# Performance work log

Hardware: AMD Instinct MI355X
Metric: run time of the kernel (lower is better)

## Reference

```python
import jax, jax.numpy as jnp
import numpy as np

N = 100000      # num_nodes
E = 1600000     # num_edges (avg degree 16)
EMB = 128       # emb_dim
HID = 128       # hidden_size
REPR = 64       # repr_dim


def setup_inputs() -> dict:
    key = jax.random.key(0)
    k0, k1, k2, k3 = jax.random.split(key, 4)
    edge_index = jax.random.randint(k0, (2, E), 0, N)
    node_emb = jax.random.normal(k1, (N, EMB), jnp.float32) * 0.1
    # GCNConv weights: glorot-like init, bias zeros (PyG default)
    W1 = jax.random.normal(k2, (EMB, HID), jnp.float32) * (1.0 / np.sqrt(EMB))
    b1 = jnp.zeros((HID,), jnp.float32)
    W2 = jax.random.normal(k3, (HID, REPR), jnp.float32) * (1.0 / np.sqrt(HID))
    b2 = jnp.zeros((REPR,), jnp.float32)
    return {"edge_index": edge_index, "node_emb": node_emb,
            "W1": W1, "b1": b1, "W2": W2, "b2": b2}


def reference(edge_index, node_emb, W1, b1, W2, b2):
    # PyG GCNConv: add self-loops, symmetric degree normalization,
    # out = scatter_add(norm * (x W)[src] -> dst) + b
    loops = jnp.arange(N, dtype=edge_index.dtype)
    src = jnp.concatenate([edge_index[0], loops])  # [E+N]
    dst = jnp.concatenate([edge_index[1], loops])
    deg = jax.ops.segment_sum(jnp.ones_like(src, dtype=node_emb.dtype), dst,
                              num_segments=N)
    dinv = jax.lax.rsqrt(deg)  # deg >= 1 thanks to self-loops
    norm = dinv[src] * dinv[dst]  # [E+N]

    def gcn_conv(x, W, b):
        h = x @ W                                   # [N, out]
        msg = norm[:, None] * h[src]                # gather + scale, [E+N, out]
        return jax.ops.segment_sum(msg, dst, num_segments=N) + b

    x = jax.nn.relu(gcn_conv(node_emb, W1, b1))
    # F.dropout(training=False) is identity in eval mode
    return gcn_conv(x, W2, b2)
```

## Files before the change

kernel.cpp:

```cpp
#include <hip/hip_runtime.h>
#include <hip/hip_bf16.h>
#include <stdint.h>


static constexpr int KD = 128;
static constexpr int BSH = 9;
static constexpr int MAXB = 256;
static constexpr int CHUNK = 8192;
static constexpr int CAP = 12288;

typedef short bf16x8 __attribute__((ext_vector_type(8)));
typedef float f32x4  __attribute__((ext_vector_type(4)));
typedef float f32x2  __attribute__((ext_vector_type(2)));

__device__ __forceinline__ unsigned short f2bf(float f) {
    __hip_bfloat16 b = __float2bfloat16(f);
    return *reinterpret_cast<unsigned short*>(&b);
}
__device__ __forceinline__ float bflo(unsigned v) { return __uint_as_float(v << 16); }
__device__ __forceinline__ float bfhi(unsigned v) { return __uint_as_float(v & 0xffff0000u); }
__device__ __forceinline__ unsigned pk2(float lo, float hi) {
    return (unsigned)f2bf(lo) | ((unsigned)f2bf(hi) << 16);
}
__device__ __forceinline__ void accp(f32x2* a, uint4 v) {
    f32x2 t;
    t.x = bflo(v.x); t.y = bfhi(v.x); a[0] += t;
    t.x = bflo(v.y); t.y = bfhi(v.y); a[1] += t;
    t.x = bflo(v.z); t.y = bfhi(v.z); a[2] += t;
    t.x = bflo(v.w); t.y = bfhi(v.w); a[3] += t;
}

__global__ __launch_bounds__(256) void init_misc(const float* __restrict__ W1,
        const float* __restrict__ W2, unsigned short* __restrict__ Wt1,
        unsigned short* __restrict__ Wt2, int* __restrict__ bcur, int nbuck) {
    int t = blockIdx.x * 256 + threadIdx.x;
    if (t < 128 * 128) {
        int k = t >> 7, nn = t & 127;
        Wt1[nn * 128 + k] = f2bf(W1[t]);
    } else if (t < 128 * 128 + 128 * 64) {
        int i = t - 128 * 128;
        int k = i >> 6, nn = i & 63;
        Wt2[nn * 128 + k] = f2bf(W2[i]);
    } else if (t < 128 * 128 + 128 * 64 + MAXB) {
        int b = t - (128 * 128 + 128 * 64);
        bcur[b] = b * CAP;
    }
}

__global__ __launch_bounds__(256) void multisplit(const int* __restrict__ src,
        const int* __restrict__ dst, int* __restrict__ bcur,
        int* __restrict__ packed, int e, int nbuck) {
    __shared__ int cnt[MAXB], lbase[MAXB], wbase[MAXB], vcnt[MAXB], scanbuf[256];
    __shared__ int buf[CHUNK];
    const int t = threadIdx.x;
    const int e0 = blockIdx.x * CHUNK;
    const int m = min(CHUNK, e - e0);

    for (int i = t; i < nbuck; i += 256) cnt[i] = 0;
    __syncthreads();
    for (int i = t; i < m; i += 256) atomicAdd(&cnt[dst[e0 + i] >> BSH], 1);
    __syncthreads();
    int v = (t < nbuck) ? cnt[t] : 0;
    scanbuf[t] = v;
    __syncthreads();
    for (int off = 1; off < 256; off <<= 1) {
        int u = (t >= off) ? scanbuf[t - off] : 0;
        __syncthreads();
        scanbuf[t] += u;
        __syncthreads();
    }
    int excl = scanbuf[t] - v;
    if (t < nbuck) {
        lbase[t] = excl;
        vcnt[t] = v;
        wbase[t] = v ? atomicAdd(&bcur[t], v) : 0;
        cnt[t] = excl;
    }
    __syncthreads();
    for (int i = t; i < m; i += 256) {
        int d = dst[e0 + i], s = src[e0 + i];
        int b = d >> BSH;
        int p = atomicAdd(&cnt[b], 1);
        buf[p] = ((d & ((1 << BSH) - 1)) << 22) | s;
    }
    __syncthreads();
    int wv = t >> 6, ln = t & 63;
    for (int b = wv; b < nbuck; b += 4) {
        int c = vcnt[b], st = lbase[b], g = wbase[b];
        int end = min(c, (b + 1) * CAP - g);
        for (int i = ln; i < end; i += 64) packed[g + i] = buf[st + i];
    }
}

__global__ __launch_bounds__(256) void bucket_build(const int* __restrict__ packed,
        const int* __restrict__ bcur, int* __restrict__ roff, int* __restrict__ degN,
        float* __restrict__ dinv, int* __restrict__ csr, int n) {
    __shared__ int deg[1 << BSH];
    __shared__ int cur[1 << BSH];
    __shared__ int wsum[4];
    const int t = threadIdx.x;
    const int b = blockIdx.x;
    const int nodeBase = b << BSH;
    const int nn = min(1 << BSH, n - nodeBase);
    const int e0 = b * CAP, e1 = bcur[b];

    for (int i = t; i < (1 << BSH); i += 256) deg[i] = 0;
    __syncthreads();
    for (int i = e0 + t; i < e1; i += 256)
        atomicAdd(&deg[(unsigned)packed[i] >> 22], 1);
    __syncthreads();

    const int i0 = t * 2;
    int d0 = deg[i0], d1 = deg[i0 + 1];
    int tsum = d0 + d1;
    int lane = t & 63, wv = t >> 6;
    int v = tsum;
    for (int off = 1; off < 64; off <<= 1) {
        int u = __shfl_up(v, off, 64);
        if (lane >= off) v += u;
    }
    if (lane == 63) wsum[wv] = v;
    __syncthreads();
    int woff = 0;
    for (int i = 0; i < wv; ++i) woff += wsum[i];
    int excl = v - tsum + woff;
    int p0 = excl, p1 = excl + d0;
    cur[i0] = p0; cur[i0 + 1] = p1;
    if (i0 < nn) {
        roff[nodeBase + i0] = e0 + p0;
        degN[nodeBase + i0] = d0;
        dinv[nodeBase + i0] = rsqrtf((float)(d0 + 1));
    }
    if (i0 + 1 < nn) {
        roff[nodeBase + i0 + 1] = e0 + p1;
        degN[nodeBase + i0 + 1] = d1;
        dinv[nodeBase + i0 + 1] = rsqrtf((float)(d1 + 1));
    }
    __syncthreads();

    for (int i = e0 + t; i < e1; i += 256) {
        unsigned pk = (unsigned)packed[i];
        int dl = pk >> 22;
        int s = pk & 0x3FFFFF;
        int slot = atomicAdd(&cur[dl], 1);
        csr[e0 + slot] = s;
    }
}

template<int C, bool XBF>
__global__ __launch_bounds__(256) void gemm_mfma(const void* __restrict__ xv,
        const unsigned short* __restrict__ Wt, const float* __restrict__ dinv,
        unsigned short* __restrict__ out, int n)
{
    constexpr int KP = KD + 8;
    constexpr int WP = 64 + 8;
    __shared__ __align__(16) unsigned short xt[64 * KP];
    __shared__ __align__(16) unsigned short lw[C * WP];
    const int t = threadIdx.x;
    const int w = t >> 6, lane = t & 63;
    const int quad = lane >> 4, l16 = lane & 15;
    const int row0 = blockIdx.x * 64;

    for (int i = t; i < 64 * 32; i += 256) {
        int r = i >> 5, c4 = (i & 31) * 4;
        int row = row0 + r;
        ushort4 pk = make_ushort4(0, 0, 0, 0);
        if (row < n) {
            if constexpr (XBF) {
                pk = *reinterpret_cast<const ushort4*>(
                    &((const unsigned short*)xv)[(size_t)row * KD + c4]);
            } else {
                float4 v = *reinterpret_cast<const float4*>(
                    &((const float*)xv)[(size_t)row * KD + c4]);
                pk.x = f2bf(v.x); pk.y = f2bf(v.y); pk.z = f2bf(v.z); pk.w = f2bf(v.w);
            }
        }
        *reinterpret_cast<ushort4*>(&xt[r * KP + c4]) = pk;
    }

    f32x4 acc[C / 16];
#pragma unroll
    for (int i = 0; i < C / 16; ++i) acc[i] = (f32x4)(0.f);

    for (int h = 0; h < 2; ++h) {
        __syncthreads();
        for (int i = t; i < C * 16; i += 256) {
            int nr = i >> 4, j = (i & 15) * 4;
            *reinterpret_cast<ushort4*>(&lw[nr * WP + j]) =
                *reinterpret_cast<const ushort4*>(&Wt[nr * KD + h * 64 + j]);
        }
        __syncthreads();
#pragma unroll
        for (int kt = 0; kt < 2; ++kt) {
            bf16x8 af = *reinterpret_cast<const bf16x8*>(
                &xt[(w * 16 + l16) * KP + h * 64 + kt * 32 + quad * 8]);
#pragma unroll
            for (int ct = 0; ct < C / 16; ++ct) {
                bf16x8 bfr = *reinterpret_cast<const bf16x8*>(
                    &lw[(ct * 16 + l16) * WP + kt * 32 + quad * 8]);
                acc[ct] = __builtin_amdgcn_mfma_f32_16x16x32_bf16(af, bfr, acc[ct], 0, 0, 0);
            }
        }
    }

#pragma unroll
    for (int j = 0; j < 4; ++j) {
        int row = row0 + w * 16 + quad * 4 + j;
        if (row < n) {
            float s = dinv[row];
#pragma unroll
            for (int ct = 0; ct < C / 16; ++ct)
                out[(size_t)row * C + ct * 16 + l16] = f2bf(acc[ct][j] * s);
        }
    }
}

__global__ __launch_bounds__(256) void gather128(const uint4* __restrict__ H,
        const int* __restrict__ roff, const int* __restrict__ degN,
        const int* __restrict__ csr, const float* __restrict__ dinv,
        const float* __restrict__ b, uint4* __restrict__ out, int n)
{
    int wid = (blockIdx.x * 256 + threadIdx.x) >> 6;
    int lane = threadIdx.x & 63;
    if (wid >= n) return;
    const int qw = lane >> 4, cp = lane & 15;
    const char* Hb = (const char*)H;
    const unsigned cpo = (unsigned)cp * 16u;
    f32x2 a[4], c[4];
#pragma unroll
    for (int i = 0; i < 4; ++i) { a[i] = (f32x2)(0.f); c[i] = (f32x2)(0.f); }
    int e0 = roff[wid], e1 = e0 + degN[wid];
    for (int base = e0; base < e1; base += 64) {
        int m = e1 - base; if (m > 64) m = 64;
        int idx = (lane < m) ? csr[base + lane] : 0;
        int j = 0;
        for (; j + 8 <= m; j += 8) {
            unsigned u0 = (unsigned)__shfl(idx, j + qw);
            unsigned u1 = (unsigned)__shfl(idx, j + 4 + qw);
            uint4 v0 = *(const uint4*)(Hb + ((u0 << 8) + cpo));
            uint4 v1 = *(const uint4*)(Hb + ((u1 << 8) + cpo));
            accp(a, v0);
            accp(c, v1);
        }
        for (; j + 4 <= m; j += 4) {
            unsigned u = (unsigned)__shfl(idx, j + qw);
            uint4 v = *(const uint4*)(Hb + ((u << 8) + cpo));
            accp(a, v);
        }
        int r = m - j;
        if (r) {
            unsigned u = (unsigned)__shfl(idx, min(j + qw, m - 1));
            if (qw < r) {
                uint4 v = *(const uint4*)(Hb + ((u << 8) + cpo));
                accp(a, v);
            }
        }
    }
#pragma unroll
    for (int i = 0; i < 4; ++i) a[i] += c[i];
#pragma unroll
    for (int i = 0; i < 4; ++i) {
        a[i].x += __shfl_xor(a[i].x, 16, 64);
        a[i].x += __shfl_xor(a[i].x, 32, 64);
        a[i].y += __shfl_xor(a[i].y, 16, 64);
        a[i].y += __shfl_xor(a[i].y, 32, 64);
    }
    if (qw == 0) {
        uint4 sv = *(const uint4*)(Hb + (((unsigned)wid << 8) + cpo));
        accp(a, sv);
        float s = dinv[wid];
        float4 b0 = ((const float4*)b)[cp * 2];
        float4 b1 = ((const float4*)b)[cp * 2 + 1];
        float r0 = fmaxf(s * a[0].x + b0.x, 0.f), r1 = fmaxf(s * a[0].y + b0.y, 0.f);
        float r2 = fmaxf(s * a[1].x + b0.z, 0.f), r3 = fmaxf(s * a[1].y + b0.w, 0.f);
        float r4 = fmaxf(s * a[2].x + b1.x, 0.f), r5 = fmaxf(s * a[2].y + b1.y, 0.f);
        float r6 = fmaxf(s * a[3].x + b1.z, 0.f), r7 = fmaxf(s * a[3].y + b1.w, 0.f);
        uint4 o;
        o.x = pk2(r0, r1); o.y = pk2(r2, r3); o.z = pk2(r4, r5); o.w = pk2(r6, r7);
        out[(size_t)wid * 16 + cp] = o;
    }
}

__global__ __launch_bounds__(256) void gather64(const uint4* __restrict__ H,
        const int* __restrict__ roff, const int* __restrict__ degN,
        const int* __restrict__ csr, const float* __restrict__ dinv,
        const float* __restrict__ b, float4* __restrict__ out, int n)
{
    int wid = (blockIdx.x * 256 + threadIdx.x) >> 6;
    int lane = threadIdx.x & 63;
    if (wid >= n) return;
    const int oc = lane >> 3, cp = lane & 7;
    const char* Hb = (const char*)H;
    const unsigned cpo = (unsigned)cp * 16u;
    f32x2 a[4], c[4];
#pragma unroll
    for (int i = 0; i < 4; ++i) { a[i] = (f32x2)(0.f); c[i] = (f32x2)(0.f); }
    int e0 = roff[wid], e1 = e0 + degN[wid];
    for (int base = e0; base < e1; base += 64) {
        int m = e1 - base; if (m > 64) m = 64;
        int idx = (lane < m) ? csr[base + lane] : 0;
        int j = 0;
        for (; j + 16 <= m; j += 16) {
            unsigned u0 = (unsigned)__shfl(idx, j + oc);
            unsigned u1 = (unsigned)__shfl(idx, j + 8 + oc);
            uint4 v0 = *(const uint4*)(Hb + ((u0 << 7) + cpo));
            uint4 v1 = *(const uint4*)(Hb + ((u1 << 7) + cpo));
            accp(a, v0);
            accp(c, v1);
        }
        for (; j + 8 <= m; j += 8) {
            unsigned u = (unsigned)__shfl(idx, j + oc);
            uint4 v = *(const uint4*)(Hb + ((u << 7) + cpo));
            accp(a, v);
        }
        int r = m - j;
        if (r) {
            unsigned u = (unsigned)__shfl(idx, min(j + oc, m - 1));
            if (oc < r) {
                uint4 v = *(const uint4*)(Hb + ((u << 7) + cpo));
                accp(a, v);
            }
        }
    }
#pragma unroll
    for (int i = 0; i < 4; ++i) a[i] += c[i];
#pragma unroll
    for (int i = 0; i < 4; ++i) {
        a[i].x += __shfl_xor(a[i].x, 8, 64);
        a[i].x += __shfl_xor(a[i].x, 16, 64);
        a[i].x += __shfl_xor(a[i].x, 32, 64);
        a[i].y += __shfl_xor(a[i].y, 8, 64);
        a[i].y += __shfl_xor(a[i].y, 16, 64);
        a[i].y += __shfl_xor(a[i].y, 32, 64);
    }
    if (oc == 0) {
        uint4 sv = *(const uint4*)(Hb + (((unsigned)wid << 7) + cpo));
        accp(a, sv);
        float s = dinv[wid];
        float4 b0 = ((const float4*)b)[cp * 2];
        float4 b1 = ((const float4*)b)[cp * 2 + 1];
        float4 o0 = make_float4(s * a[0].x + b0.x, s * a[0].y + b0.y,
                                s * a[1].x + b0.z, s * a[1].y + b0.w);
        float4 o1 = make_float4(s * a[2].x + b1.x, s * a[2].y + b1.y,
                                s * a[3].x + b1.z, s * a[3].y + b1.w);
        out[(size_t)wid * 16 + cp * 2] = o0;
        out[(size_t)wid * 16 + cp * 2 + 1] = o1;
    }
}

extern "C" void kernel_launch(void* const* d_in, const int* in_sizes, int n_in,
                              void* d_out, int out_size, void* d_ws, size_t ws_size,
                              hipStream_t stream)
{
    const int* ei = (const int*)d_in[0];
    const int E = in_sizes[0] / 2;
    const float* emb = (const float*)d_in[1];
    const int N = in_sizes[1] / KD;
    const float* W1 = (const float*)d_in[2];
    const float* b1 = (const float*)d_in[3];
    const float* W2 = (const float*)d_in[4];
    const float* b2 = (const float*)d_in[5];
    const int* src = ei;
    const int* dst = ei + E;
    const int nbuck = (N + (1 << BSH) - 1) >> BSH;

    char* p = (char*)d_ws;
    auto alloc = [&](size_t bytes) { char* q = p; p += (bytes + 255) & ~(size_t)255; return q; };
    unsigned short* h1 = (unsigned short*)alloc((size_t)N * 128 * sizeof(unsigned short));
    unsigned short* x2 = (unsigned short*)alloc((size_t)N * 128 * sizeof(unsigned short));
    int*   csr    = (int*)  alloc((size_t)nbuck * CAP * sizeof(int));
    int*   packed = (int*)  alloc((size_t)nbuck * CAP * sizeof(int));
    int*   roff   = (int*)  alloc((size_t)N * sizeof(int));
    int*   degN   = (int*)  alloc((size_t)N * sizeof(int));
    float* dinv   = (float*)alloc((size_t)N * sizeof(float));
    int*   bcur   = (int*)  alloc(MAXB * sizeof(int));
    unsigned short* Wt1 = (unsigned short*)alloc(128 * 128 * sizeof(unsigned short));
    unsigned short* Wt2 = (unsigned short*)alloc(64 * 128 * sizeof(unsigned short));
    unsigned short* h2 = h1;

    init_misc<<<97, 256, 0, stream>>>(W1, W2, Wt1, Wt2, bcur, nbuck);
    multisplit<<<(E + CHUNK - 1) / CHUNK, 256, 0, stream>>>(src, dst, bcur, packed, E, nbuck);
    bucket_build<<<nbuck, 256, 0, stream>>>(packed, bcur, roff, degN, dinv, csr, N);

    gemm_mfma<128, false><<<(N + 63) / 64, 256, 0, stream>>>(emb, Wt1, dinv, h1, N);
    gather128<<<(N + 3) / 4, 256, 0, stream>>>((const uint4*)h1, roff, degN, csr,
                                               dinv, b1, (uint4*)x2, N);

    gemm_mfma<64, true><<<(N + 63) / 64, 256, 0, stream>>>(x2, Wt2, dinv, h2, N);
    gather64<<<(N + 3) / 4, 256, 0, stream>>>((const uint4*)h2, roff, degN, csr,
                                              dinv, b2, (float4*)d_out, N);
}
```

Before: 296.8 us.

## Fuse layer-1 gather with layer-2 GEMM via shared-memory tile; halve multisplit chunk

The layer-1 neighbour aggregation (with bias and ReLU) now writes its bf16 rows into a shared-memory tile, and the same block then runs the layer-2 MFMA GEMM on that tile. This removes the x2 intermediate round trip through global memory and one kernel launch. In exchange, each wave now processes 16 rows in sequence instead of one, which lowers parallelism and latency hiding for the gather phase. The multisplit chunk size is also halved, which doubles the number of blocks in that kernel.

Result: slower. 313.3 us (+5.6%).

```diff
diff --git a/kernel.cpp b/kernel.cpp
--- a/kernel.cpp
+++ b/kernel.cpp
@@ -6,7 +6,7 @@
 static constexpr int KD = 128;
 static constexpr int BSH = 9;
 static constexpr int MAXB = 256;
-static constexpr int CHUNK = 8192;
+static constexpr int CHUNK = 4096;
 static constexpr int CAP = 12288;
 
 typedef short bf16x8 __attribute__((ext_vector_type(8)));
@@ -147,11 +147,11 @@
     }
 }
 
-template<int C, bool XBF>
-__global__ __launch_bounds__(256) void gemm_mfma(const void* __restrict__ xv,
+__global__ __launch_bounds__(256) void gemm_mfma128(const float* __restrict__ xv,
         const unsigned short* __restrict__ Wt, const float* __restrict__ dinv,
         unsigned short* __restrict__ out, int n)
 {
+    constexpr int C = 128;
     constexpr int KP = KD + 8;
     constexpr int WP = 64 + 8;
     __shared__ __align__(16) unsigned short xt[64 * KP];
@@ -166,14 +166,8 @@
         int row = row0 + r;
         ushort4 pk = make_ushort4(0, 0, 0, 0);
         if (row < n) {
-            if constexpr (XBF) {
-                pk = *reinterpret_cast<const ushort4*>(
-                    &((const unsigned short*)xv)[(size_t)row * KD + c4]);
-            } else {
-                float4 v = *reinterpret_cast<const float4*>(
-                    &((const float*)xv)[(size_t)row * KD + c4]);
-                pk.x = f2bf(v.x); pk.y = f2bf(v.y); pk.z = f2bf(v.z); pk.w = f2bf(v.w);
-            }
+            float4 v = *reinterpret_cast<const float4*>(&xv[(size_t)row * KD + c4]);
+            pk.x = f2bf(v.x); pk.y = f2bf(v.y); pk.z = f2bf(v.z); pk.w = f2bf(v.w);
         }
         *reinterpret_cast<ushort4*>(&xt[r * KP + c4]) = pk;
     }
@@ -215,69 +209,119 @@
     }
 }
 
-__global__ __launch_bounds__(256) void gather128(const uint4* __restrict__ H,
+__global__ __launch_bounds__(256) void gather_gemm64(const uint4* __restrict__ H,
         const int* __restrict__ roff, const int* __restrict__ degN,
         const int* __restrict__ csr, const float* __restrict__ dinv,
-        const float* __restrict__ b, uint4* __restrict__ out, int n)
+        const float* __restrict__ b, const unsigned short* __restrict__ Wt2,
+        unsigned short* __restrict__ h2, int n)
 {
-    int wid = (blockIdx.x * 256 + threadIdx.x) >> 6;
-    int lane = threadIdx.x & 63;
-    if (wid >= n) return;
+    constexpr int KP = KD + 8;
+    constexpr int WP = 64 + 8;
+    __shared__ __align__(16) unsigned short xt[64 * KP];
+    __shared__ __align__(16) unsigned short lw[64 * WP];
+    const int t = threadIdx.x;
+    const int w = t >> 6, lane = t & 63;
     const int qw = lane >> 4, cp = lane & 15;
+    const int row0 = blockIdx.x * 64;
     const char* Hb = (const char*)H;
     const unsigned cpo = (unsigned)cp * 16u;
-    f32x2 a[4], c[4];
-#pragma unroll
-    for (int i = 0; i < 4; ++i) { a[i] = (f32x2)(0.f); c[i] = (f32x2)(0.f); }
-    int e0 = roff[wid], e1 = e0 + degN[wid];
-    for (int base = e0; base < e1; base += 64) {
-        int m = e1 - base; if (m > 64) m = 64;
-        int idx = (lane < m) ? csr[base + lane] : 0;
-        int j = 0;
-        for (; j + 8 <= m; j += 8) {
-            unsigned u0 = (unsigned)__shfl(idx, j + qw);
-            unsigned u1 = (unsigned)__shfl(idx, j + 4 + qw);
-            uint4 v0 = *(const uint4*)(Hb + ((u0 << 8) + cpo));
-            uint4 v1 = *(const uint4*)(Hb + ((u1 << 8) + cpo));
-            accp(a, v0);
-            accp(c, v1);
-        }
-        for (; j + 4 <= m; j += 4) {
-            unsigned u = (unsigned)__shfl(idx, j + qw);
-            uint4 v = *(const uint4*)(Hb + ((u << 8) + cpo));
-            accp(a, v);
-        }
-        int r = m - j;
-        if (r) {
-            unsigned u = (unsigned)__shfl(idx, min(j + qw, m - 1));
-            if (qw < r) {
-                uint4 v = *(const uint4*)(Hb + ((u << 8) + cpo));
-                accp(a, v);
-            }
-        }
-    }
-#pragma unroll
-    for (int i = 0; i < 4; ++i) a[i] += c[i];
-#pragma unroll
-    for (int i = 0; i < 4; ++i) {
-        a[i].x += __shfl_xor(a[i].x, 16, 64);
-        a[i].x += __shfl_xor(a[i].x, 32, 64);
-        a[i].y += __shfl_xor(a[i].y, 16, 64);
-        a[i].y += __shfl_xor(a[i].y, 32, 64);
-    }
-    if (qw == 0) {
-        uint4 sv = *(const uint4*)(Hb + (((unsigned)wid << 8) + cpo));
-        accp(a, sv);
-        float s = dinv[wid];
-        float4 b0 = ((const float4*)b)[cp * 2];
-        float4 b1 = ((const float4*)b)[cp * 2 + 1];
-        float r0 = fmaxf(s * a[0].x + b0.x, 0.f), r1 = fmaxf(s * a[0].y + b0.y, 0.f);
-        float r2 = fmaxf(s * a[1].x + b0.z, 0.f), r3 = fmaxf(s * a[1].y + b0.w, 0.f);
-        float r4 = fmaxf(s * a[2].x + b1.x, 0.f), r5 = fmaxf(s * a[2].y + b1.y, 0.f);
-        float r6 = fmaxf(s * a[3].x + b1.z, 0.f), r7 = fmaxf(s * a[3].y + b1.w, 0.f);
-        uint4 o;
-        o.x = pk2(r0, r1); o.y = pk2(r2, r3); o.z = pk2(r4, r5); o.w = pk2(r6, r7);
-        out[(size_t)wid * 16 + cp] = o;
+
+    for (int rr = 0; rr < 16; ++rr) {
+        const int r = w * 16 + rr;
+        const int wid = row0 + r;
+        f32x2 a[4], c[4];
+#pragma unroll
+        for (int i = 0; i < 4; ++i) { a[i] = (f32x2)(0.f); c[i] = (f32x2)(0.f); }
+        if (wid < n) {
+            int e0 = roff[wid], e1 = e0 + degN[wid];
+            for (int base = e0; base < e1; base += 64) {
+                int m = e1 - base; if (m > 64) m = 64;
+                int idx = (lane < m) ? csr[base + lane] : 0;
+                int j = 0;
+                for (; j + 8 <= m; j += 8) {
+                    unsigned u0 = (unsigned)__shfl(idx, j + qw);
+                    unsigned u1 = (unsigned)__shfl(idx, j + 4 + qw);
+                    uint4 v0 = *(const uint4*)(Hb + ((u0 << 8) + cpo));
+                    uint4 v1 = *(const uint4*)(Hb + ((u1 << 8) + cpo));
+                    accp(a, v0);
+                    accp(c, v1);
+                }
+                for (; j + 4 <= m; j += 4) {
+                    unsigned u = (unsigned)__shfl(idx, j + qw);
+                    uint4 v = *(const uint4*)(Hb + ((u << 8) + cpo));
+                    accp(a, v);
+                }
+                int rm = m - j;
+                if (rm) {
+                    unsigned u = (unsigned)__shfl(idx, min(j + qw, m - 1));
+                    if (qw < rm) {
+                        uint4 v = *(const uint4*)(Hb + ((u << 8) + cpo));
+                        accp(a, v);
+                    }
+                }
+            }
+#pragma unroll
+            for (int i = 0; i < 4; ++i) a[i] += c[i];
+#pragma unroll
+            for (int i = 0; i < 4; ++i) {
+                a[i].x += __shfl_xor(a[i].x, 16, 64);
+                a[i].x += __shfl_xor(a[i].x, 32, 64);
+                a[i].y += __shfl_xor(a[i].y, 16, 64);
+                a[i].y += __shfl_xor(a[i].y, 32, 64);
+            }
+            if (qw == 0) {
+                uint4 sv = *(const uint4*)(Hb + (((unsigned)wid << 8) + cpo));
+                accp(a, sv);
+                float s = dinv[wid];
+                float4 b0 = ((const float4*)b)[cp * 2];
+                float4 b1 = ((const float4*)b)[cp * 2 + 1];
+                float r0 = fmaxf(s * a[0].x + b0.x, 0.f), r1 = fmaxf(s * a[0].y + b0.y, 0.f);
+                float r2 = fmaxf(s * a[1].x + b0.z, 0.f), r3 = fmaxf(s * a[1].y + b0.w, 0.f);
+                float r4 = fmaxf(s * a[2].x + b1.x, 0.f), r5 = fmaxf(s * a[2].y + b1.y, 0.f);
+                float r6 = fmaxf(s * a[3].x + b1.z, 0.f), r7 = fmaxf(s * a[3].y + b1.w, 0.f);
+                uint4 o;
+                o.x = pk2(r0, r1); o.y = pk2(r2, r3); o.z = pk2(r4, r5); o.w = pk2(r6, r7);
+                *reinterpret_cast<uint4*>(&xt[r * KP + cp * 8]) = o;
+            }
+        } else if (qw == 0) {
+            *reinterpret_cast<uint4*>(&xt[r * KP + cp * 8]) = make_uint4(0, 0, 0, 0);
+        }
+    }
+
+    f32x4 acc[4];
+#pragma unroll
+    for (int i = 0; i < 4; ++i) acc[i] = (f32x4)(0.f);
+
+    for (int h = 0; h < 2; ++h) {
+        __syncthreads();
+        for (int i = t; i < 64 * 16; i += 256) {
+            int nr = i >> 4, j = (i & 15) * 4;
+            *reinterpret_cast<ushort4*>(&lw[nr * WP + j]) =
+                *reinterpret_cast<const ushort4*>(&Wt2[nr * KD + h * 64 + j]);
+        }
+        __syncthreads();
+#pragma unroll
+        for (int kt = 0; kt < 2; ++kt) {
+            bf16x8 af = *reinterpret_cast<const bf16x8*>(
+                &xt[(w * 16 + cp) * KP + h * 64 + kt * 32 + qw * 8]);
+#pragma unroll
+            for (int ct = 0; ct < 4; ++ct) {
+                bf16x8 bfr = *reinterpret_cast<const bf16x8*>(
+                    &lw[(ct * 16 + cp) * WP + kt * 32 + qw * 8]);
+                acc[ct] = __builtin_amdgcn_mfma_f32_16x16x32_bf16(af, bfr, acc[ct], 0, 0, 0);
+            }
+        }
+    }
+
+#pragma unroll
+    for (int j = 0; j < 4; ++j) {
+        int row = row0 + w * 16 + qw * 4 + j;
+        if (row < n) {
+            float s = dinv[row];
+#pragma unroll
+            for (int ct = 0; ct < 4; ++ct)
+                h2[(size_t)row * 64 + ct * 16 + cp] = f2bf(acc[ct][j] * s);
+        }
     }
 }
 
@@ -367,7 +411,7 @@
     char* p = (char*)d_ws;
     auto alloc = [&](size_t bytes) { char* q = p; p += (bytes + 255) & ~(size_t)255; return q; };
     unsigned short* h1 = (unsigned short*)alloc((size_t)N * 128 * sizeof(unsigned short));
-    unsigned short* x2 = (unsigned short*)alloc((size_t)N * 128 * sizeof(unsigned short));
+    unsigned short* h2 = (unsigned short*)alloc((size_t)N * 64 * sizeof(unsigned short));
     int*   csr    = (int*)  alloc((size_t)nbuck * CAP * sizeof(int));
     int*   packed = (int*)  alloc((size_t)nbuck * CAP * sizeof(int));
     int*   roff   = (int*)  alloc((size_t)N * sizeof(int));
@@ -376,17 +420,16 @@
     int*   bcur   = (int*)  alloc(MAXB * sizeof(int));
     unsigned short* Wt1 = (unsigned short*)alloc(128 * 128 * sizeof(unsigned short));
     unsigned short* Wt2 = (unsigned short*)alloc(64 * 128 * sizeof(unsigned short));
-    unsigned short* h2 = h1;
 
     init_misc<<<97, 256, 0, stream>>>(W1, W2, Wt1, Wt2, bcur, nbuck);
     multisplit<<<(E + CHUNK - 1) / CHUNK, 256, 0, stream>>>(src, dst, bcur, packed, E, nbuck);
     bucket_build<<<nbuck, 256, 0, stream>>>(packed, bcur, roff, degN, dinv, csr, N);
 
-    gemm_mfma<128, false><<<(N + 63) / 64, 256, 0, stream>>>(emb, Wt1, dinv, h1, N);
-    gather128<<<(N + 3) / 4, 256, 0, stream>>>((const uint4*)h1, roff, degN, csr,
-                                               dinv, b1, (uint4*)x2, N);
-
-    gemm_mfma<64, true><<<(N + 63) / 64, 256, 0, stream>>>(x2, Wt2, dinv, h2, N);
+    gemm_mfma128<<<(N + 63) / 64, 256, 0, stream>>>(emb, Wt1, dinv, h1, N);
+
+    gather_gemm64<<<(N + 63) / 64, 256, 0, stream>>>((const uint4*)h1, roff, degN, csr,
+                                                     dinv, b1, Wt2, h2, N);
+
     gather64<<<(N + 3) / 4, 256, 0, stream>>>((const uint4*)h2, roff, degN, csr,
                                               dinv, b2, (float4*)d_out, N);
 }
```

## Replace atomic multisplit with histogram-scan-scatter and split layer-1 gather launch

Applied to the files above, without the earlier changes.

The single multisplit kernel, which reserved each chunk's output space with global atomics and staged edges in shared memory, becomes three kernels. A per-chunk bucket histogram is followed by a per-bucket exclusive scan across chunks and a direct scatter into packed using the precomputed offsets. Chunks shrink from 8192 to 2048 edges, giving more blocks and a deterministic edge order, at the cost of two extra launches and a global histogram array. The layer-1 gather is also split into two launches over node halves, which adds launch overhead with no clear benefit.

Result: no change. 302.7 us (+2.0%).

```diff
diff --git a/kernel.cpp b/kernel.cpp
--- a/kernel.cpp
+++ b/kernel.cpp
@@ -6,7 +6,7 @@
 static constexpr int KD = 128;
 static constexpr int BSH = 9;
 static constexpr int MAXB = 256;
-static constexpr int CHUNK = 8192;
+static constexpr int CHUNK = 2048;
 static constexpr int CAP = 12288;
 
 typedef short bf16x8 __attribute__((ext_vector_type(8)));
@@ -32,7 +32,7 @@
 
 __global__ __launch_bounds__(256) void init_misc(const float* __restrict__ W1,
         const float* __restrict__ W2, unsigned short* __restrict__ Wt1,
-        unsigned short* __restrict__ Wt2, int* __restrict__ bcur, int nbuck) {
+        unsigned short* __restrict__ Wt2) {
     int t = blockIdx.x * 256 + threadIdx.x;
     if (t < 128 * 128) {
         int k = t >> 7, nn = t & 127;
@@ -41,54 +41,65 @@
         int i = t - 128 * 128;
         int k = i >> 6, nn = i & 63;
         Wt2[nn * 128 + k] = f2bf(W2[i]);
-    } else if (t < 128 * 128 + 128 * 64 + MAXB) {
-        int b = t - (128 * 128 + 128 * 64);
-        bcur[b] = b * CAP;
-    }
-}
-
-__global__ __launch_bounds__(256) void multisplit(const int* __restrict__ src,
-        const int* __restrict__ dst, int* __restrict__ bcur,
-        int* __restrict__ packed, int e, int nbuck) {
-    __shared__ int cnt[MAXB], lbase[MAXB], wbase[MAXB], vcnt[MAXB], scanbuf[256];
-    __shared__ int buf[CHUNK];
+    }
+}
+
+__global__ __launch_bounds__(256) void chunk_hist(const int* __restrict__ dst,
+        int* __restrict__ ghist, int e, int nbuck) {
+    __shared__ int cnt[MAXB];
     const int t = threadIdx.x;
     const int e0 = blockIdx.x * CHUNK;
     const int m = min(CHUNK, e - e0);
-
     for (int i = t; i < nbuck; i += 256) cnt[i] = 0;
     __syncthreads();
     for (int i = t; i < m; i += 256) atomicAdd(&cnt[dst[e0 + i] >> BSH], 1);
     __syncthreads();
-    int v = (t < nbuck) ? cnt[t] : 0;
-    scanbuf[t] = v;
-    __syncthreads();
-    for (int off = 1; off < 256; off <<= 1) {
-        int u = (t >= off) ? scanbuf[t - off] : 0;
+    for (int i = t; i < nbuck; i += 256) ghist[blockIdx.x * nbuck + i] = cnt[i];
+}
+
+__global__ __launch_bounds__(256) void chunk_scan(int* __restrict__ ghist,
+        int* __restrict__ bcur, int nchunk, int nbuck) {
+    __shared__ int wsum[4];
+    const int t = threadIdx.x;
+    const int b = blockIdx.x;
+    const int lane = t & 63, wv = t >> 6;
+    int carry = 0;
+    for (int t0 = 0; t0 < nchunk; t0 += 256) {
+        int c = t0 + t;
+        int v = (c < nchunk) ? ghist[c * nbuck + b] : 0;
+        int iv = v;
+        for (int off = 1; off < 64; off <<= 1) {
+            int u = __shfl_up(iv, off, 64);
+            if (lane >= off) iv += u;
+        }
+        if (lane == 63) wsum[wv] = iv;
         __syncthreads();
-        scanbuf[t] += u;
+        int woff = 0;
+        for (int i = 0; i < wv; ++i) woff += wsum[i];
+        int total = wsum[0] + wsum[1] + wsum[2] + wsum[3];
+        int excl = iv - v + woff;
+        if (c < nchunk) ghist[c * nbuck + b] = b * CAP + carry + excl;
+        carry += total;
         __syncthreads();
     }
-    int excl = scanbuf[t] - v;
-    if (t < nbuck) {
-        lbase[t] = excl;
-        vcnt[t] = v;
-        wbase[t] = v ? atomicAdd(&bcur[t], v) : 0;
-        cnt[t] = excl;
-    }
+    if (t == 0) bcur[b] = b * CAP + carry;
+}
+
+__global__ __launch_bounds__(256) void chunk_scatter(const int* __restrict__ src,
+        const int* __restrict__ dst, const int* __restrict__ ghist,
+        int* __restrict__ packed, int e, int nbuck) {
+    __shared__ int cur[MAXB];
+    const int t = threadIdx.x;
+    const int e0 = blockIdx.x * CHUNK;
+    const int m = min(CHUNK, e - e0);
+    for (int i = t; i < nbuck; i += 256) cur[i] = ghist[blockIdx.x * nbuck + i];
     __syncthreads();
     for (int i = t; i < m; i += 256) {
         int d = dst[e0 + i], s = src[e0 + i];
         int b = d >> BSH;
-        int p = atomicAdd(&cnt[b], 1);
-        buf[p] = ((d & ((1 << BSH) - 1)) << 22) | s;
-    }
-    __syncthreads();
-    int wv = t >> 6, ln = t & 63;
-    for (int b = wv; b < nbuck; b += 4) {
-        int c = vcnt[b], st = lbase[b], g = wbase[b];
-        int end = min(c, (b + 1) * CAP - g);
-        for (int i = ln; i < end; i += 64) packed[g + i] = buf[st + i];
+        int p = atomicAdd(&cur[b], 1);
+        if (p < (b + 1) * CAP)
+            packed[p] = ((d & ((1 << BSH) - 1)) << 22) | s;
     }
 }
 
@@ -218,11 +229,11 @@
 __global__ __launch_bounds__(256) void gather128(const uint4* __restrict__ H,
         const int* __restrict__ roff, const int* __restrict__ degN,
         const int* __restrict__ csr, const float* __restrict__ dinv,
-        const float* __restrict__ b, uint4* __restrict__ out, int n)
+        const float* __restrict__ b, uint4* __restrict__ out, int n0, int n1)
 {
-    int wid = (blockIdx.x * 256 + threadIdx.x) >> 6;
+    int wid = n0 + ((blockIdx.x * 256 + threadIdx.x) >> 6);
     int lane = threadIdx.x & 63;
-    if (wid >= n) return;
+    if (wid >= n1) return;
     const int qw = lane >> 4, cp = lane & 15;
     const char* Hb = (const char*)H;
     const unsigned cpo = (unsigned)cp * 16u;
@@ -363,6 +374,7 @@
     const int* src = ei;
     const int* dst = ei + E;
     const int nbuck = (N + (1 << BSH) - 1) >> BSH;
+    const int nchunk = (E + CHUNK - 1) / CHUNK;
 
     char* p = (char*)d_ws;
     auto alloc = [&](size_t bytes) { char* q = p; p += (bytes + 255) & ~(size_t)255; return q; };
@@ -370,6 +382,7 @@
     unsigned short* x2 = (unsigned short*)alloc((size_t)N * 128 * sizeof(unsigned short));
     int*   csr    = (int*)  alloc((size_t)nbuck * CAP * sizeof(int));
     int*   packed = (int*)  alloc((size_t)nbuck * CAP * sizeof(int));
+    int*   ghist  = (int*)  alloc((size_t)nchunk * nbuck * sizeof(int));
     int*   roff   = (int*)  alloc((size_t)N * sizeof(int));
     int*   degN   = (int*)  alloc((size_t)N * sizeof(int));
     float* dinv   = (float*)alloc((size_t)N * sizeof(float));
@@ -378,13 +391,18 @@
     unsigned short* Wt2 = (unsigned short*)alloc(64 * 128 * sizeof(unsigned short));
     unsigned short* h2 = h1;
 
-    init_misc<<<97, 256, 0, stream>>>(W1, W2, Wt1, Wt2, bcur, nbuck);
-    multisplit<<<(E + CHUNK - 1) / CHUNK, 256, 0, stream>>>(src, dst, bcur, packed, E, nbuck);
+    init_misc<<<96, 256, 0, stream>>>(W1, W2, Wt1, Wt2);
+    chunk_hist<<<nchunk, 256, 0, stream>>>(dst, ghist, E, nbuck);
+    chunk_scan<<<nbuck, 256, 0, stream>>>(ghist, bcur, nchunk, nbuck);
+    chunk_scatter<<<nchunk, 256, 0, stream>>>(src, dst, ghist, packed, E, nbuck);
     bucket_build<<<nbuck, 256, 0, stream>>>(packed, bcur, roff, degN, dinv, csr, N);
 
     gemm_mfma<128, false><<<(N + 63) / 64, 256, 0, stream>>>(emb, Wt1, dinv, h1, N);
-    gather128<<<(N + 3) / 4, 256, 0, stream>>>((const uint4*)h1, roff, degN, csr,
-                                               dinv, b1, (uint4*)x2, N);
+    const int half = ((N / 2) + 63) & ~63;
+    gather128<<<half / 4, 256, 0, stream>>>((const uint4*)h1, roff, degN, csr,
+                                            dinv, b1, (uint4*)x2, 0, half);
+    gather128<<<(N - half + 3) / 4, 256, 0, stream>>>((const uint4*)h1, roff, degN, csr,
+                                                      dinv, b1, (uint4*)x2, half, N);
 
     gemm_mfma<64, true><<<(N + 63) / 64, 256, 0, stream>>>(x2, Wt2, dinv, h2, N);
     gather64<<<(N + 3) / 4, 256, 0, stream>>>((const uint4*)h2, roff, degN, csr,
```
